# Kernel optimization log

Measured on AMD Instinct MI355X. Metric: run time of the kernel, lower is better.

The kernel has to match this reference:

```python
import jax, jax.numpy as jnp
import numpy as np

E = 1024      # embed_dim
H = 16        # num_heads
D = E // H    # head_dim
F = 4096      # ff_dim
EPS = 1e-5


def setup_inputs() -> dict:
    key = jax.random.key(0)
    ks = jax.random.split(key, 12)
    s = 0.02
    return {
        "x": jax.random.normal(ks[0], (2, 2048, E), dtype=jnp.float32),
        "qkv_w": jax.random.normal(ks[1], (3 * E, E), dtype=jnp.float32) * s,
        "qkv_b": jnp.zeros((3 * E,), dtype=jnp.float32),
        "out_w": jax.random.normal(ks[2], (E, E), dtype=jnp.float32) * s,
        "out_b": jnp.zeros((E,), dtype=jnp.float32),
        "ff1_w": jax.random.normal(ks[3], (F, E), dtype=jnp.float32) * s,
        "ff1_b": jnp.zeros((F,), dtype=jnp.float32),
        "ff2_w": jax.random.normal(ks[4], (E, F), dtype=jnp.float32) * s,
        "ff2_b": jnp.zeros((E,), dtype=jnp.float32),
        "ln1_g": jnp.ones((E,), dtype=jnp.float32),
        "ln1_b": jnp.zeros((E,), dtype=jnp.float32),
        "ln2_g": jnp.ones((E,), dtype=jnp.float32),
        "ln2_b": jnp.zeros((E,), dtype=jnp.float32),
    }


def _layernorm(x, g, b):
    mu = jnp.mean(x, axis=-1, keepdims=True)
    var = jnp.mean(jnp.square(x - mu), axis=-1, keepdims=True)
    return (x - mu) * jax.lax.rsqrt(var + EPS) * g + b


def reference(x, qkv_w, qkv_b, out_w, out_b, ff1_w, ff1_b, ff2_w, ff2_b,
              ln1_g, ln1_b, ln2_g, ln2_b):
    B, S, _ = x.shape
    scale = D ** -0.5

    # --- attention sublayer (pre-LN) ---
    h = _layernorm(x, ln1_g, ln1_b)
    qkv = h @ qkv_w.T + qkv_b                          # [B,S,3E]
    qkv = qkv.reshape(B, S, 3, H, D)
    q, k, v = qkv[:, :, 0], qkv[:, :, 1], qkv[:, :, 2]  # [B,S,H,D]
    scores = jnp.einsum("bqhd,bkhd->bhqk", q, k) * scale
    attn = jax.nn.softmax(scores, axis=-1)
    o = jnp.einsum("bhqk,bkhd->bqhd", attn, v).reshape(B, S, E)
    x = x + o @ out_w.T + out_b

    # --- FFN sublayer (pre-LN, exact GELU) ---
    h = _layernorm(x, ln2_g, ln2_b)
    h = jax.nn.gelu(h @ ff1_w.T + ff1_b, approximate=False)
    x = x + h @ ff2_w.T + ff2_b
    return x
```

## Files before the change

### kernel.cpp

```cpp
#include <hip/hip_runtime.h>
#include <math.h>


typedef __attribute__((ext_vector_type(8))) short short8;
typedef __attribute__((ext_vector_type(4))) float f32x4;

__device__ __forceinline__ unsigned short f2bf(float f) {
  unsigned int u = __float_as_uint(f);
  u += 0x7fffu + ((u >> 16) & 1u);
  return (unsigned short)(u >> 16);
}

__device__ __forceinline__ short8 pack8(float4 a, float4 b) {
  short8 p;
  p[0] = (short)f2bf(a.x); p[1] = (short)f2bf(a.y);
  p[2] = (short)f2bf(a.z); p[3] = (short)f2bf(a.w);
  p[4] = (short)f2bf(b.x); p[5] = (short)f2bf(b.y);
  p[6] = (short)f2bf(b.z); p[7] = (short)f2bf(b.w);
  return p;
}

__device__ __forceinline__ float gelu_fast(float v) {
  float g = 0.7978845608f * fmaf(0.044715f * v, v * v, v);
  float den = 1.0f + exp2f(-2.885390082f * g);
  return v * __builtin_amdgcn_rcpf(den);
}

__device__ __forceinline__ void async16(const void* g, void* l) {
  __builtin_amdgcn_global_load_lds(
      (const __attribute__((address_space(1))) unsigned int*)g,
      (__attribute__((address_space(3))) unsigned int*)l, 16, 0, 0);
}

__global__ __launch_bounds__(256) void conv_all(
    const float* __restrict__ i0, unsigned short* __restrict__ o0, int n0,
    const float* __restrict__ i1, unsigned short* __restrict__ o1, int n1,
    const float* __restrict__ i2, unsigned short* __restrict__ o2, int n2,
    const float* __restrict__ i3, unsigned short* __restrict__ o3, int n3) {
  int i = blockIdx.x * 256 + threadIdx.x;
  const float* in; unsigned short* out;
  if (i < n0) { in = i0; out = o0; }
  else if ((i -= n0) < n1) { in = i1; out = o1; }
  else if ((i -= n1) < n2) { in = i2; out = o2; }
  else { i -= n2; in = i3; out = o3; if (i >= n3) return; }
  float4 v = ((const float4*)in)[i];
  ushort4 u;
  u.x = f2bf(v.x); u.y = f2bf(v.y); u.z = f2bf(v.z); u.w = f2bf(v.w);
  ((ushort4*)out)[i] = u;
}

__global__ __launch_bounds__(256) void ln_kernel(const float* __restrict__ x,
                                                 const float* __restrict__ g,
                                                 const float* __restrict__ b,
                                                 unsigned short* __restrict__ out) {
  int row = blockIdx.x;
  int t = threadIdx.x;
  const float4* x4 = (const float4*)(x + (size_t)row * 1024);
  float4 v = x4[t];
  float s1 = v.x + v.y + v.z + v.w;
  float s2 = v.x * v.x + v.y * v.y + v.z * v.z + v.w * v.w;
  for (int off = 1; off < 64; off <<= 1) {
    s1 += __shfl_xor(s1, off, 64);
    s2 += __shfl_xor(s2, off, 64);
  }
  __shared__ float r1[4], r2[4];
  int w = t >> 6, lane = t & 63;
  if (lane == 0) { r1[w] = s1; r2[w] = s2; }
  __syncthreads();
  s1 = r1[0] + r1[1] + r1[2] + r1[3];
  s2 = r2[0] + r2[1] + r2[2] + r2[3];
  float mu = s1 * (1.0f / 1024.0f);
  float var = s2 * (1.0f / 1024.0f) - mu * mu;
  float rstd = rsqrtf(var + 1e-5f);
  int c = t * 4;
  float4 gv = ((const float4*)g)[t];
  float4 bv = ((const float4*)b)[t];
  unsigned short* o = out + (size_t)row * 1024 + c;
  o[0] = f2bf((v.x - mu) * rstd * gv.x + bv.x);
  o[1] = f2bf((v.y - mu) * rstd * gv.y + bv.y);
  o[2] = f2bf((v.z - mu) * rstd * gv.z + bv.z);
  o[3] = f2bf((v.w - mu) * rstd * gv.w + bv.w);
}

template <int MODE, int BM, int BK, int LIN>
__global__ __launch_bounds__(256) void gemm_bt(
    const unsigned short* __restrict__ A, const unsigned short* __restrict__ W,
    const float* __restrict__ bias, int M, int N, int K,
    const float* __restrict__ resid, float* __restrict__ out_f32,
    unsigned short* __restrict__ out_bf16,
    unsigned short* __restrict__ qbp, unsigned short* __restrict__ kbp,
    unsigned short* __restrict__ vtb) {
  constexpr int MI = BM / 32;
  constexpr int LPR = BK / 8;
  constexpr int RPW = 512 / BK;
  constexpr int RRND = 2048 / BK;
  constexpr int NIA = BM / RRND;
  constexpr int NIW = 128 / RRND;
  constexpr int KK = BK / 32;
  __shared__ __attribute__((aligned(16))) unsigned short As[2][BM * BK];
  __shared__ __attribute__((aligned(16))) unsigned short Ws[2][128 * BK];
  int tid = threadIdx.x;
  int w = tid >> 6, lane = tid & 63, quad = lane >> 4, l16 = lane & 15;
  int wrow = w >> 1, wcol = w & 1;
  int m0, n0;
  if (LIN) {
    int id = blockIdx.x;
    int mc = M / BM;
    m0 = (id % mc) * BM;
    n0 = (id / mc) * 128;
  } else {
    m0 = blockIdx.y * BM;
    n0 = blockIdx.x * 128;
  }

  int srow = lane / LPR;
  int sseg = lane % LPR;
  int ssw = (BK == 64) ? (srow & 7) : ((srow >> 1) & 3);
  int scol = (sseg ^ ssw) * 8;
  const unsigned short* Ag = A + (size_t)(m0 + w * RPW + srow) * K + scol;
  const unsigned short* Wg = W + (size_t)(n0 + w * RPW + srow) * K + scol;

  f32x4 acc[MI][4] = {};

  for (int i = 0; i < NIA; i++)
    async16(Ag + (size_t)(i * RRND) * K, As[0] + (i * RRND + w * RPW) * BK);
  for (int i = 0; i < NIW; i++)
    async16(Wg + (size_t)(i * RRND) * K, Ws[0] + (i * RRND + w * RPW) * BK);

  int fsw = (BK == 64) ? (l16 & 7) : ((l16 >> 1) & 3);

  for (int k0 = 0; k0 < K; k0 += BK) {
    int buf = (k0 / BK) & 1;
    __syncthreads();
    if (k0 + BK < K) {
      int nb = buf ^ 1;
      for (int i = 0; i < NIA; i++)
        async16(Ag + (size_t)(i * RRND) * K + k0 + BK, As[nb] + (i * RRND + w * RPW) * BK);
      for (int i = 0; i < NIW; i++)
        async16(Wg + (size_t)(i * RRND) * K + k0 + BK, Ws[nb] + (i * RRND + w * RPW) * BK);
    }
    short8 af[MI][KK], bf[4][KK];
    for (int i = 0; i < MI; i++)
      for (int kk = 0; kk < KK; kk++)
        af[i][kk] = *(const short8*)(As[buf] + (wrow * (BM / 2) + i * 16 + l16) * BK +
                                     ((kk * 4 + quad) ^ fsw) * 8);
    for (int j = 0; j < 4; j++)
      for (int kk = 0; kk < KK; kk++)
        bf[j][kk] = *(const short8*)(Ws[buf] + (wcol * 64 + j * 16 + l16) * BK +
                                     ((kk * 4 + quad) ^ fsw) * 8);
    for (int kk = 0; kk < KK; kk++)
      for (int i = 0; i < MI; i++)
        for (int j = 0; j < 4; j++)
          acc[i][j] = __builtin_amdgcn_mfma_f32_16x16x32_bf16(af[i][kk], bf[j][kk], acc[i][j], 0, 0, 0);
  }

  __syncthreads();
  float* ep = (w < 2) ? ((float*)As + w * 1024) : ((float*)Ws + (w - 2) * 1024);
  int orow = lane >> 2;
  int oseg = lane & 3;
  int colbase = n0 + wcol * 64;
  float bv[4];
  for (int j = 0; j < 4; j++) bv[j] = bias[colbase + j * 16 + l16];

  if (MODE == 1 || MODE == 2) {
    for (int i = 0; i < MI; i++) {
      for (int j = 0; j < 4; j++)
        for (int r = 0; r < 4; r++) {
          int row = quad * 4 + r, col = j * 16 + l16;
          float v = acc[i][j][r] + bv[j];
          if (MODE == 2) v = gelu_fast(v);
          ep[row * 64 + (((col >> 2) ^ (row & 7)) << 2) + (col & 3)] = v;
        }
      asm volatile("s_waitcnt lgkmcnt(0)" ::: "memory");
      int grow = m0 + wrow * (BM / 2) + i * 16 + orow;
      if (MODE == 1) {
        for (int t = 0; t < 4; t++) {
          int sl = t * 4 + oseg;
          float4 v = *(float4*)(ep + orow * 64 + ((sl ^ (orow & 7)) << 2));
          const float4 rv = *(const float4*)(resid + (size_t)grow * N + colbase + sl * 4);
          v.x += rv.x; v.y += rv.y; v.z += rv.z; v.w += rv.w;
          *(float4*)(out_f32 + (size_t)grow * N + colbase + sl * 4) = v;
        }
      } else {
        for (int t = 0; t < 2; t++) {
          int s0 = t * 8 + oseg * 2;
          float4 a = *(float4*)(ep + orow * 64 + ((s0 ^ (orow & 7)) << 2));
          float4 b = *(float4*)(ep + orow * 64 + (((s0 + 1) ^ (orow & 7)) << 2));
          *(short8*)(out_bf16 + (size_t)grow * N + colbase + t * 32 + oseg * 8) = pack8(a, b);
        }
      }
      asm volatile("s_waitcnt lgkmcnt(0)" ::: "memory");
    }
  } else {
    int whichW = colbase >> 10;
    int hh = (colbase & 1023) >> 6;
    int bh = (m0 >> 11) * 16 + hh;
    int sbase = (m0 & 2047) + wrow * (BM / 2);
    if (whichW < 2) {
      unsigned short* dst0 = (whichW == 0) ? qbp : kbp;
      for (int i = 0; i < MI; i++) {
        for (int j = 0; j < 4; j++)
          for (int r = 0; r < 4; r++) {
            int row = quad * 4 + r, col = j * 16 + l16;
            ep[row * 64 + (((col >> 2) ^ (row & 7)) << 2) + (col & 3)] = acc[i][j][r] + bv[j];
          }
        asm volatile("s_waitcnt lgkmcnt(0)" ::: "memory");
        int s = sbase + i * 16 + orow;
        for (int t = 0; t < 2; t++) {
          int s0 = t * 8 + oseg * 2;
          float4 a = *(float4*)(ep + orow * 64 + ((s0 ^ (orow & 7)) << 2));
          float4 b = *(float4*)(ep + orow * 64 + (((s0 + 1) ^ (orow & 7)) << 2));
          *(short8*)(dst0 + ((size_t)bh * 2048 + s) * 64 + t * 32 + oseg * 8) = pack8(a, b);
        }
        asm volatile("s_waitcnt lgkmcnt(0)" ::: "memory");
      }
    } else {
      for (int j = 0; j < 4; j++) {
        for (int i = 0; i < MI; i++) {
          float4 v4;
          v4.x = acc[i][j][0] + bv[j];
          v4.y = acc[i][j][1] + bv[j];
          v4.z = acc[i][j][2] + bv[j];
          v4.w = acc[i][j][3] + bv[j];
          *(float4*)(ep + l16 * 64 + (((i * 4 + quad) ^ (l16 & 7)) << 2)) = v4;
        }
        asm volatile("s_waitcnt lgkmcnt(0)" ::: "memory");
        int d = j * 16 + orow;
        for (int t = 0; t < 2; t++) {
          int s0 = t * 8 + oseg * 2;
          float4 a = *(float4*)(ep + orow * 64 + ((s0 ^ (orow & 7)) << 2));
          float4 b = *(float4*)(ep + orow * 64 + (((s0 + 1) ^ (orow & 7)) << 2));
          *(short8*)(vtb + ((size_t)bh * 64 + d) * 2048 + sbase + t * 32 + oseg * 8) = pack8(a, b);
        }
        asm volatile("s_waitcnt lgkmcnt(0)" ::: "memory");
      }
    }
  }
}

#define ALDP 72

__global__ __launch_bounds__(256) void attn_kernel(const unsigned short* __restrict__ qb,
                                                   const unsigned short* __restrict__ kb,
                                                   const unsigned short* __restrict__ vtb,
                                                   unsigned short* __restrict__ ob) {
  __shared__ __attribute__((aligned(16))) unsigned short Ks[2][64 * 64];
  __shared__ __attribute__((aligned(16))) unsigned short Vs[2][64 * 64];
  __shared__ __attribute__((aligned(16))) unsigned short Ps[4][2 * 16 * ALDP];

  int tid = threadIdx.x;
  int w = tid >> 6, lane = tid & 63, quad = lane >> 4, l16 = lane & 15;
  int bi = blockIdx.x;
  int bh = (bi & 7) * 4 + ((bi >> 3) & 3);
  int q0 = (bi >> 5) * 128 + w * 32;

  const unsigned short* qbase = qb + ((size_t)bh * 2048 + q0) * 64;
  const unsigned short* kbase = kb + (size_t)bh * 2048 * 64;
  const unsigned short* vbase = vtb + (size_t)bh * 64 * 2048;
  unsigned short* Pw = Ps[w];

  int srow = lane >> 3;
  int scol = ((lane & 7) ^ srow) * 8;
  const unsigned short* kg0 = kbase + (size_t)(w * 16 + srow) * 64 + scol;
  const unsigned short* kg1 = kbase + (size_t)(w * 16 + 8 + srow) * 64 + scol;
  const unsigned short* vg0 = vbase + (size_t)(w * 16 + srow) * 2048 + scol;
  const unsigned short* vg1 = vbase + (size_t)(w * 16 + 8 + srow) * 2048 + scol;

  short8 qf[2][2];
  for (int u = 0; u < 2; u++) {
    qf[u][0] = *(const short8*)(qbase + (u * 16 + l16) * 64 + quad * 8);
    qf[u][1] = *(const short8*)(qbase + (u * 16 + l16) * 64 + 32 + quad * 8);
  }

  float l0 = 0.0f, l1 = 0.0f;
  f32x4 oacc[2][4] = {};
  const float sc2 = 0.125f * 1.44269504089f;
  int sw = l16 & 7;

  async16(kg0, &Ks[0][(w * 16) * 64]);
  async16(kg1, &Ks[0][(w * 16 + 8) * 64]);
  async16(vg0, &Vs[0][(w * 16) * 64]);
  async16(vg1, &Vs[0][(w * 16 + 8) * 64]);

  for (int c0 = 0; c0 < 2048; c0 += 64) {
    int buf = (c0 >> 6) & 1;
    __syncthreads();
    if (c0 + 64 < 2048) {
      int nb = buf ^ 1;
      async16(kg0 + (size_t)(c0 + 64) * 64, &Ks[nb][(w * 16) * 64]);
      async16(kg1 + (size_t)(c0 + 64) * 64, &Ks[nb][(w * 16 + 8) * 64]);
      async16(vg0 + c0 + 64, &Vs[nb][(w * 16) * 64]);
      async16(vg1 + c0 + 64, &Vs[nb][(w * 16 + 8) * 64]);
    }
    short8 kf[4][2];
    for (int t = 0; t < 4; t++) {
      const unsigned short* kr = &Ks[buf][(t * 16 + l16) * 64];
      kf[t][0] = *(const short8*)(kr + (quad ^ sw) * 8);
      kf[t][1] = *(const short8*)(kr + ((4 + quad) ^ sw) * 8);
    }
    f32x4 s[2][4];
    for (int u = 0; u < 2; u++)
      for (int t = 0; t < 4; t++) {
        f32x4 z = {0.0f, 0.0f, 0.0f, 0.0f};
        z = __builtin_amdgcn_mfma_f32_16x16x32_bf16(kf[t][0], qf[u][0], z, 0, 0, 0);
        z = __builtin_amdgcn_mfma_f32_16x16x32_bf16(kf[t][1], qf[u][1], z, 0, 0, 0);
        s[u][t] = z;
      }
    for (int u = 0; u < 2; u++) {
      float rsum = 0.0f;
      unsigned short* pr = Pw + (u * 16 + l16) * ALDP;
      for (int t = 0; t < 4; t++) {
        float p0 = exp2f(s[u][t][0] * sc2);
        float p1 = exp2f(s[u][t][1] * sc2);
        float p2 = exp2f(s[u][t][2] * sc2);
        float p3 = exp2f(s[u][t][3] * sc2);
        rsum += (p0 + p1) + (p2 + p3);
        uint2 pk;
        pk.x = __builtin_amdgcn_perm(__float_as_uint(p1), __float_as_uint(p0), 0x07060302u);
        pk.y = __builtin_amdgcn_perm(__float_as_uint(p3), __float_as_uint(p2), 0x07060302u);
        *(uint2*)(pr + t * 16 + quad * 4) = pk;
      }
      rsum += __shfl_xor(rsum, 16, 64);
      rsum += __shfl_xor(rsum, 32, 64);
      if (u == 0) l0 += rsum; else l1 += rsum;
    }
    asm volatile("s_waitcnt lgkmcnt(0)" ::: "memory");
    for (int ks = 0; ks < 2; ks++) {
      short8 af0 = *(const short8*)(Pw + l16 * ALDP + ks * 32 + quad * 8);
      short8 af1 = *(const short8*)(Pw + (16 + l16) * ALDP + ks * 32 + quad * 8);
      for (int j = 0; j < 4; j++) {
        short8 vf = *(const short8*)(&Vs[buf][(j * 16 + l16) * 64] +
                                     ((ks * 4 + quad) ^ sw) * 8);
        oacc[0][j] = __builtin_amdgcn_mfma_f32_16x16x32_bf16(af0, vf, oacc[0][j], 0, 0, 0);
        oacc[1][j] = __builtin_amdgcn_mfma_f32_16x16x32_bf16(af1, vf, oacc[1][j], 0, 0, 0);
      }
    }
  }

  float linv[2][4];
  for (int u = 0; u < 2; u++) {
    float lr = (u == 0) ? l0 : l1;
    for (int r = 0; r < 4; r++) linv[u][r] = 1.0f / __shfl(lr, quad * 4 + r, 64);
  }
  int bb = bh >> 4, hh = bh & 15;
  for (int u = 0; u < 2; u++)
    for (int j = 0; j < 4; j++)
      for (int r = 0; r < 4; r++) {
        size_t tok = (size_t)bb * 2048 + q0 + u * 16 + quad * 4 + r;
        ob[tok * 1024 + hh * 64 + j * 16 + l16] = f2bf(oacc[u][j][r] * linv[u][r]);
      }
}

extern "C" void kernel_launch(void* const* d_in, const int* in_sizes, int n_in,
                              void* d_out, int out_size, void* d_ws, size_t ws_size,
                              hipStream_t stream) {
  (void)in_sizes; (void)n_in; (void)out_size; (void)ws_size;
  const float* x     = (const float*)d_in[0];
  const float* qkv_w = (const float*)d_in[1];
  const float* qkv_b = (const float*)d_in[2];
  const float* out_w = (const float*)d_in[3];
  const float* out_b = (const float*)d_in[4];
  const float* ff1_w = (const float*)d_in[5];
  const float* ff1_b = (const float*)d_in[6];
  const float* ff2_w = (const float*)d_in[7];
  const float* ff2_b = (const float*)d_in[8];
  const float* ln1_g = (const float*)d_in[9];
  const float* ln1_b = (const float*)d_in[10];
  const float* ln2_g = (const float*)d_in[11];
  const float* ln2_b = (const float*)d_in[12];
  float* out = (float*)d_out;
  char* ws = (char*)d_ws;

  const int M = 4096;

  unsigned short* WQ = (unsigned short*)(ws + 0);
  unsigned short* WO = (unsigned short*)(ws + 6291456);
  unsigned short* W1 = (unsigned short*)(ws + 8388608);
  unsigned short* W2 = (unsigned short*)(ws + 16777216);
  unsigned short* Hb = (unsigned short*)(ws + 25165824);
  unsigned short* Qb = (unsigned short*)(ws + 33554432);
  unsigned short* Kb = (unsigned short*)(ws + 41943040);
  unsigned short* VT = (unsigned short*)(ws + 50331648);
  unsigned short* Ob = (unsigned short*)(ws + 58720256);
  float*          X1 = (float*)(ws + 67108864);
  unsigned short* Gb = (unsigned short*)(ws + 33554432);

  conv_all<<<12288, 256, 0, stream>>>(qkv_w, WQ, 786432, out_w, WO, 262144,
                                      ff1_w, W1, 1048576, ff2_w, W2, 1048576);

  ln_kernel<<<4096, 256, 0, stream>>>(x, ln1_g, ln1_b, Hb);

  gemm_bt<0, 128, 32, 0><<<dim3(24, 32), 256, 0, stream>>>(
      Hb, WQ, qkv_b, M, 3072, 1024, nullptr, nullptr, nullptr, Qb, Kb, VT);

  attn_kernel<<<512, 256, 0, stream>>>(Qb, Kb, VT, Ob);

  gemm_bt<1, 64, 64, 1><<<512, 256, 0, stream>>>(
      Ob, WO, out_b, M, 1024, 1024, x, X1, nullptr, nullptr, nullptr, nullptr);

  ln_kernel<<<4096, 256, 0, stream>>>(X1, ln2_g, ln2_b, Hb);

  gemm_bt<2, 128, 32, 0><<<dim3(32, 32), 256, 0, stream>>>(
      Hb, W1, ff1_b, M, 4096, 1024, nullptr, nullptr, Gb, nullptr, nullptr, nullptr);

  gemm_bt<1, 64, 64, 1><<<512, 256, 0, stream>>>(
      Gb, W2, ff2_b, M, 1024, 4096, X1, out, nullptr, nullptr, nullptr, nullptr);
}
```

Baseline: 353.8 us.

## Use 8 waves of 16 query rows per attention block; fold softmax scale into Q

The attention kernel now launches 512 threads per block. Each of 8 waves handles 16 query rows instead of 4 waves with 32 rows, and each wave loads half as many K/V rows into shared memory. The softmax scale and log2e factor are folded into Q in the QKV GEMM epilogue, so the attention loop no longer multiplies scores before exp2. The intent is more waves in flight for latency hiding and less work per score. In exchange, each wave reuses its K fragments over half as many query rows, and the larger blocks may lower occupancy per CU.

```diff
diff --git a/kernel.cpp b/kernel.cpp
--- a/kernel.cpp
+++ b/kernel.cpp
@@ -198,11 +198,13 @@
     int sbase = (m0 & 2047) + wrow * (BM / 2);
     if (whichW < 2) {
       unsigned short* dst0 = (whichW == 0) ? qbp : kbp;
+      float qs = (whichW == 0) ? 0.1803368801f : 1.0f;
       for (int i = 0; i < MI; i++) {
         for (int j = 0; j < 4; j++)
           for (int r = 0; r < 4; r++) {
             int row = quad * 4 + r, col = j * 16 + l16;
-            ep[row * 64 + (((col >> 2) ^ (row & 7)) << 2) + (col & 3)] = acc[i][j][r] + bv[j];
+            ep[row * 64 + (((col >> 2) ^ (row & 7)) << 2) + (col & 3)] =
+                (acc[i][j][r] + bv[j]) * qs;
           }
         asm volatile("s_waitcnt lgkmcnt(0)" ::: "memory");
         int s = sbase + i * 16 + orow;
@@ -240,19 +242,19 @@
 
 #define ALDP 72
 
-__global__ __launch_bounds__(256) void attn_kernel(const unsigned short* __restrict__ qb,
+__global__ __launch_bounds__(512) void attn_kernel(const unsigned short* __restrict__ qb,
                                                    const unsigned short* __restrict__ kb,
                                                    const unsigned short* __restrict__ vtb,
                                                    unsigned short* __restrict__ ob) {
   __shared__ __attribute__((aligned(16))) unsigned short Ks[2][64 * 64];
   __shared__ __attribute__((aligned(16))) unsigned short Vs[2][64 * 64];
-  __shared__ __attribute__((aligned(16))) unsigned short Ps[4][2 * 16 * ALDP];
+  __shared__ __attribute__((aligned(16))) unsigned short Ps[8][16 * ALDP];
 
   int tid = threadIdx.x;
   int w = tid >> 6, lane = tid & 63, quad = lane >> 4, l16 = lane & 15;
   int bi = blockIdx.x;
   int bh = (bi & 7) * 4 + ((bi >> 3) & 3);
-  int q0 = (bi >> 5) * 128 + w * 32;
+  int q0 = (bi >> 5) * 128 + w * 16;
 
   const unsigned short* qbase = qb + ((size_t)bh * 2048 + q0) * 64;
   const unsigned short* kbase = kb + (size_t)bh * 2048 * 64;
@@ -261,36 +263,27 @@
 
   int srow = lane >> 3;
   int scol = ((lane & 7) ^ srow) * 8;
-  const unsigned short* kg0 = kbase + (size_t)(w * 16 + srow) * 64 + scol;
-  const unsigned short* kg1 = kbase + (size_t)(w * 16 + 8 + srow) * 64 + scol;
-  const unsigned short* vg0 = vbase + (size_t)(w * 16 + srow) * 2048 + scol;
-  const unsigned short* vg1 = vbase + (size_t)(w * 16 + 8 + srow) * 2048 + scol;
-
-  short8 qf[2][2];
-  for (int u = 0; u < 2; u++) {
-    qf[u][0] = *(const short8*)(qbase + (u * 16 + l16) * 64 + quad * 8);
-    qf[u][1] = *(const short8*)(qbase + (u * 16 + l16) * 64 + 32 + quad * 8);
-  }
-
-  float l0 = 0.0f, l1 = 0.0f;
-  f32x4 oacc[2][4] = {};
-  const float sc2 = 0.125f * 1.44269504089f;
+  const unsigned short* kg0 = kbase + (size_t)(w * 8 + srow) * 64 + scol;
+  const unsigned short* vg0 = vbase + (size_t)(w * 8 + srow) * 2048 + scol;
+
+  short8 qf[2];
+  qf[0] = *(const short8*)(qbase + l16 * 64 + quad * 8);
+  qf[1] = *(const short8*)(qbase + l16 * 64 + 32 + quad * 8);
+
+  float lsum = 0.0f;
+  f32x4 oacc[4] = {};
   int sw = l16 & 7;
 
-  async16(kg0, &Ks[0][(w * 16) * 64]);
-  async16(kg1, &Ks[0][(w * 16 + 8) * 64]);
-  async16(vg0, &Vs[0][(w * 16) * 64]);
-  async16(vg1, &Vs[0][(w * 16 + 8) * 64]);
+  async16(kg0, &Ks[0][(w * 8) * 64]);
+  async16(vg0, &Vs[0][(w * 8) * 64]);
 
   for (int c0 = 0; c0 < 2048; c0 += 64) {
     int buf = (c0 >> 6) & 1;
     __syncthreads();
     if (c0 + 64 < 2048) {
       int nb = buf ^ 1;
-      async16(kg0 + (size_t)(c0 + 64) * 64, &Ks[nb][(w * 16) * 64]);
-      async16(kg1 + (size_t)(c0 + 64) * 64, &Ks[nb][(w * 16 + 8) * 64]);
-      async16(vg0 + c0 + 64, &Vs[nb][(w * 16) * 64]);
-      async16(vg1 + c0 + 64, &Vs[nb][(w * 16 + 8) * 64]);
+      async16(kg0 + (size_t)(c0 + 64) * 64, &Ks[nb][(w * 8) * 64]);
+      async16(vg0 + c0 + 64, &Vs[nb][(w * 8) * 64]);
     }
     short8 kf[4][2];
     for (int t = 0; t < 4; t++) {
@@ -298,57 +291,48 @@
       kf[t][0] = *(const short8*)(kr + (quad ^ sw) * 8);
       kf[t][1] = *(const short8*)(kr + ((4 + quad) ^ sw) * 8);
     }
-    f32x4 s[2][4];
-    for (int u = 0; u < 2; u++)
-      for (int t = 0; t < 4; t++) {
-        f32x4 z = {0.0f, 0.0f, 0.0f, 0.0f};
-        z = __builtin_amdgcn_mfma_f32_16x16x32_bf16(kf[t][0], qf[u][0], z, 0, 0, 0);
-        z = __builtin_amdgcn_mfma_f32_16x16x32_bf16(kf[t][1], qf[u][1], z, 0, 0, 0);
-        s[u][t] = z;
-      }
-    for (int u = 0; u < 2; u++) {
-      float rsum = 0.0f;
-      unsigned short* pr = Pw + (u * 16 + l16) * ALDP;
-      for (int t = 0; t < 4; t++) {
-        float p0 = exp2f(s[u][t][0] * sc2);
-        float p1 = exp2f(s[u][t][1] * sc2);
-        float p2 = exp2f(s[u][t][2] * sc2);
-        float p3 = exp2f(s[u][t][3] * sc2);
-        rsum += (p0 + p1) + (p2 + p3);
-        uint2 pk;
-        pk.x = __builtin_amdgcn_perm(__float_as_uint(p1), __float_as_uint(p0), 0x07060302u);
-        pk.y = __builtin_amdgcn_perm(__float_as_uint(p3), __float_as_uint(p2), 0x07060302u);
-        *(uint2*)(pr + t * 16 + quad * 4) = pk;
-      }
-      rsum += __shfl_xor(rsum, 16, 64);
-      rsum += __shfl_xor(rsum, 32, 64);
-      if (u == 0) l0 += rsum; else l1 += rsum;
-    }
+    f32x4 s[4];
+    for (int t = 0; t < 4; t++) {
+      f32x4 z = {0.0f, 0.0f, 0.0f, 0.0f};
+      z = __builtin_amdgcn_mfma_f32_16x16x32_bf16(kf[t][0], qf[0], z, 0, 0, 0);
+      z = __builtin_amdgcn_mfma_f32_16x16x32_bf16(kf[t][1], qf[1], z, 0, 0, 0);
+      s[t] = z;
+    }
+    float rsum = 0.0f;
+    unsigned short* pr = Pw + l16 * ALDP;
+    for (int t = 0; t < 4; t++) {
+      float p0 = exp2f(s[t][0]);
+      float p1 = exp2f(s[t][1]);
+      float p2 = exp2f(s[t][2]);
+      float p3 = exp2f(s[t][3]);
+      rsum += (p0 + p1) + (p2 + p3);
+      uint2 pk;
+      pk.x = __builtin_amdgcn_perm(__float_as_uint(p1), __float_as_uint(p0), 0x07060302u);
+      pk.y = __builtin_amdgcn_perm(__float_as_uint(p3), __float_as_uint(p2), 0x07060302u);
+      *(uint2*)(pr + t * 16 + quad * 4) = pk;
+    }
+    rsum += __shfl_xor(rsum, 16, 64);
+    rsum += __shfl_xor(rsum, 32, 64);
+    lsum += rsum;
     asm volatile("s_waitcnt lgkmcnt(0)" ::: "memory");
     for (int ks = 0; ks < 2; ks++) {
-      short8 af0 = *(const short8*)(Pw + l16 * ALDP + ks * 32 + quad * 8);
-      short8 af1 = *(const short8*)(Pw + (16 + l16) * ALDP + ks * 32 + quad * 8);
+      short8 af = *(const short8*)(Pw + l16 * ALDP + ks * 32 + quad * 8);
       for (int j = 0; j < 4; j++) {
         short8 vf = *(const short8*)(&Vs[buf][(j * 16 + l16) * 64] +
                                      ((ks * 4 + quad) ^ sw) * 8);
-        oacc[0][j] = __builtin_amdgcn_mfma_f32_16x16x32_bf16(af0, vf, oacc[0][j], 0, 0, 0);
-        oacc[1][j] = __builtin_amdgcn_mfma_f32_16x16x32_bf16(af1, vf, oacc[1][j], 0, 0, 0);
+        oacc[j] = __builtin_amdgcn_mfma_f32_16x16x32_bf16(af, vf, oacc[j], 0, 0, 0);
       }
     }
   }
 
-  float linv[2][4];
-  for (int u = 0; u < 2; u++) {
-    float lr = (u == 0) ? l0 : l1;
-    for (int r = 0; r < 4; r++) linv[u][r] = 1.0f / __shfl(lr, quad * 4 + r, 64);
-  }
+  float linv[4];
+  for (int r = 0; r < 4; r++) linv[r] = 1.0f / __shfl(lsum, quad * 4 + r, 64);
   int bb = bh >> 4, hh = bh & 15;
-  for (int u = 0; u < 2; u++)
-    for (int j = 0; j < 4; j++)
-      for (int r = 0; r < 4; r++) {
-        size_t tok = (size_t)bb * 2048 + q0 + u * 16 + quad * 4 + r;
-        ob[tok * 1024 + hh * 64 + j * 16 + l16] = f2bf(oacc[u][j][r] * linv[u][r]);
-      }
+  for (int j = 0; j < 4; j++)
+    for (int r = 0; r < 4; r++) {
+      size_t tok = (size_t)bb * 2048 + q0 + quad * 4 + r;
+      ob[tok * 1024 + hh * 64 + j * 16 + l16] = f2bf(oacc[j][r] * linv[r]);
+    }
 }
 
 extern "C" void kernel_launch(void* const* d_in, const int* in_sizes, int n_in,
@@ -393,7 +377,7 @@
   gemm_bt<0, 128, 32, 0><<<dim3(24, 32), 256, 0, stream>>>(
       Hb, WQ, qkv_b, M, 3072, 1024, nullptr, nullptr, nullptr, Qb, Kb, VT);
 
-  attn_kernel<<<512, 256, 0, stream>>>(Qb, Kb, VT, Ob);
+  attn_kernel<<<512, 512, 0, stream>>>(Qb, Kb, VT, Ob);
 
   gemm_bt<1, 64, 64, 1><<<512, 256, 0, stream>>>(
       Ob, WO, out_b, M, 1024, 1024, x, X1, nullptr, nullptr, nullptr, nullptr);
```

Measured after the change: 358.3 us. About the same (+1.3%).
